# Kernel tuning notes

Hardware: AMD Instinct MI355X
Metric: run time of the kernel (lower is better)

## Reference

```python
import jax, jax.numpy as jnp
import numpy as np
from jax import lax

# pywt Wavelet('db4') decomposition filters
DEC_LO = jnp.array([-0.010597401784997278, 0.032883011666982945, 0.030841381835986965,
                    -0.18703481171888114, -0.02798376941698385, 0.6308807679295904,
                    0.7148465705525415, 0.23037781330885523], dtype=jnp.float32)
DEC_HI = jnp.array([-0.23037781330885523, 0.7148465705525415, -0.6308807679295904,
                    -0.02798376941698385, 0.18703481171888114, 0.030841381835986965,
                    -0.032883011666982945, -0.010597401784997278], dtype=jnp.float32)


def dwt_level(x, lo, hi):
    # single-level pywt dwt, mode='symmetric', along last axis
    f = lo.shape[0]
    p = f - 1
    pad = [(0, 0)] * (x.ndim - 1) + [(p, p)]
    xe = jnp.pad(x, pad, mode='symmetric')[..., 1:]  # offset 1 matches pywt phase
    lead = x.shape[:-1]
    xin = xe.reshape(-1, 1, xe.shape[-1])            # [N,1,L]
    filt = jnp.stack([lo[::-1], hi[::-1]])[:, None, :]  # flip: true convolution, [2,1,f]
    out = lax.conv_general_dilated(xin, filt, (2,), 'VALID')  # [N,2,floor((n+f-1)/2)]
    cA = out[:, 0].reshape(lead + (-1,))
    cD = out[:, 1].reshape(lead + (-1,))
    return cA, cD


def wavedec4(x):
    # pywt.wavedec(x,'db4',level=4) concatenated: [cA4,cD4,cD3,cD2,cD1]
    details = []
    a = x
    for _ in range(4):
        a, d = dwt_level(a, DEC_LO, DEC_HI)
        details.append(d)
    return jnp.concatenate([a] + details[::-1], axis=-1)


def lstm_last(xs, w_ih, w_hh, b_ih, b_hh):
    # torch LSTM (gate order i,f,g,o); returns last timestep hidden state
    B, T, _ = xs.shape
    H = w_hh.shape[1]
    h0 = jnp.zeros((B, H), xs.dtype)
    c0 = jnp.zeros((B, H), xs.dtype)
    b = b_ih + b_hh

    def step(carry, x_t):
        h, c = carry
        gates = x_t @ w_ih.T + h @ w_hh.T + b
        i, f, g, o = jnp.split(gates, 4, axis=-1)
        c = jax.nn.sigmoid(f) * c + jax.nn.sigmoid(i) * jnp.tanh(g)
        h = jax.nn.sigmoid(o) * jnp.tanh(c)
        return (h, c), None

    (h, _), _ = lax.scan(step, (h0, c0), jnp.swapaxes(xs, 0, 1))
    return h


def setup_inputs() -> dict:
    key = jax.random.key(0)
    ks = jax.random.split(key, 9)
    B, S, T = 256, 1024, 21
    return {
        'x': jax.random.normal(ks[0], (B, S, T), jnp.float32),
        'conv_w': jax.random.normal(ks[1], (64, 78, 3), jnp.float32) * 0.06,
        'conv_b': jax.random.normal(ks[2], (64,), jnp.float32) * 0.06,
        'w_ih': jax.random.normal(ks[3], (128, 64), jnp.float32) * 0.12,
        'w_hh': jax.random.normal(ks[4], (128, 32), jnp.float32) * 0.17,
        'b_ih': jax.random.normal(ks[5], (128,), jnp.float32) * 0.17,
        'b_hh': jax.random.normal(ks[6], (128,), jnp.float32) * 0.17,
        'fc_w': jax.random.normal(ks[7], (1, 32), jnp.float32) * 0.17,
        'fc_b': jax.random.normal(ks[8], (1,), jnp.float32) * 0.17,
    }


def reference(x, conv_w, conv_b, w_ih, w_hh, b_ih, b_hh, fc_w, fc_b):
    freq = jnp.abs(jnp.fft.rfft(x, axis=2))          # [B,S,11]
    tf = wavedec4(x)                                 # [B,S,46]
    combined = jnp.concatenate([x, freq, tf], axis=2)  # [B,S,78]
    combined = jnp.swapaxes(combined, 1, 2)          # [B,78,S]
    y = lax.conv_general_dilated(combined, conv_w, (1,), [(1, 1)]) + conv_b[None, :, None]
    y = jax.nn.relu(y)
    B, C, S = y.shape
    y = y.reshape(B, C, S // 2, 2).max(axis=-1)      # max_pool1d(k=2,s=2)
    y = jnp.transpose(y, (0, 2, 1))                  # [B,S//2,64]
    h = lstm_last(y, w_ih, w_hh, b_ih, b_hh)         # [B,32]
    return h @ fc_w.T + fc_b                         # [B,1]
```

## Files before the change

kernel.cpp:

```cpp
#include <hip/hip_runtime.h>
#include <math.h>

typedef _Float16 half8 __attribute__((ext_vector_type(8)));
typedef __fp16 fp16x2 __attribute__((ext_vector_type(2)));
typedef float floatx16 __attribute__((ext_vector_type(16)));
typedef float float2v __attribute__((ext_vector_type(2)));

constexpr float L2E = 1.4426950408889634f;

constexpr float DLO[8] = {-0.010597401784997278f, 0.032883011666982945f, 0.030841381835986965f,
                          -0.18703481171888114f, -0.02798376941698385f, 0.6308807679295904f,
                          0.7148465705525415f, 0.23037781330885523f};
constexpr float DHI[8] = {-0.23037781330885523f, 0.7148465705525415f, -0.6308807679295904f,
                          -0.02798376941698385f, 0.18703481171888114f, 0.030841381835986965f,
                          -0.032883011666982945f, -0.010597401784997278f};

constexpr float CT21[21] = {
  1.0f,          0.95557281f,  0.82623877f,  0.62348980f,  0.36534102f,  0.07473009f,
  -0.22252093f, -0.5f,        -0.73305187f, -0.90096887f, -0.98883083f,
  -0.98883083f, -0.90096887f, -0.73305187f, -0.5f,        -0.22252093f,
  0.07473009f,   0.36534102f,  0.62348980f,  0.82623877f,  0.95557281f};
constexpr float ST21[21] = {
  0.0f,          0.29475517f,  0.56332006f,  0.78183148f,  0.93087375f,  0.99720380f,
  0.97492791f,   0.86602540f,  0.68017274f,  0.43388374f,  0.14904227f,
  -0.14904227f, -0.43388374f, -0.68017274f, -0.86602540f, -0.97492791f,
  -0.99720380f, -0.93087375f, -0.78183148f, -0.56332006f, -0.29475517f};

template<int N>
__device__ __forceinline__ void dwt_step(const float* in, float* a, float* d) {
  constexpr int NO = (N + 7) / 2;
#pragma unroll
  for (int i = 0; i < NO; i++) {
    float sa = 0.f, sd = 0.f;
#pragma unroll
    for (int j = 0; j < 8; j++) {
      int rel = 2 * i + j - 6;
      int idx = (rel < 0) ? (-rel - 1) : ((rel >= N) ? (2 * N - rel - 1) : rel);
      float v = in[idx];
      sa = fmaf(v, DLO[7 - j], sa);
      sd = fmaf(v, DHI[7 - j], sd);
    }
    a[i] = sa;
    d[i] = sd;
  }
}

__device__ __forceinline__ void gload_lds16(const void* g, void* l) {
  __builtin_amdgcn_global_load_lds(
      (const __attribute__((address_space(1))) unsigned int*)g,
      (__attribute__((address_space(3))) unsigned int*)l, 16, 0, 0);
}

__device__ __forceinline__ void feature_row(const float* __restrict__ xr,
                                            _Float16* hrow) {
  float xx[21];
#pragma unroll
  for (int t = 0; t < 21; t++) xx[t] = xr[t];

#pragma unroll
  for (int i = 78; i < 88; i++) hrow[i] = (_Float16)0.f;

#pragma unroll
  for (int t = 0; t < 21; t++) hrow[t] = (_Float16)xx[t];

#pragma unroll
  for (int k = 0; k < 11; k++) {
    float re = 0.f, im = 0.f;
#pragma unroll
    for (int t = 0; t < 21; t++) {
      const int m = (k * t) % 21;
      re = fmaf(xx[t], CT21[m], re);
      im = fmaf(xx[t], ST21[m], im);
    }
    hrow[21 + k] = (_Float16)sqrtf(re * re + im * im);
  }

  float a1[14], d1[14];
  dwt_step<21>(xx, a1, d1);
#pragma unroll
  for (int i = 0; i < 14; i++) hrow[64 + i] = (_Float16)d1[i];
  float a2[10], d2[10];
  dwt_step<14>(a1, a2, d2);
#pragma unroll
  for (int i = 0; i < 10; i++) hrow[54 + i] = (_Float16)d2[i];
  float a3[8], d3[8];
  dwt_step<10>(a2, a3, d3);
#pragma unroll
  for (int i = 0; i < 8; i++) hrow[46 + i] = (_Float16)d3[i];
  float a4[7], d4[7];
  dwt_step<8>(a3, a4, d4);
#pragma unroll
  for (int i = 0; i < 7; i++) {
    hrow[32 + i] = (_Float16)a4[i];
    hrow[39 + i] = (_Float16)d4[i];
  }
}

__global__ __launch_bounds__(256) void wprep_kernel(const float* __restrict__ cw,
                                                    const float* __restrict__ w_ih,
                                                    const float* __restrict__ b_ih,
                                                    const float* __restrict__ b_hh,
                                                    _Float16* __restrict__ WbT,
                                                    _Float16* __restrict__ wih16,
                                                    float* __restrict__ biasI) {
  int idx = blockIdx.x * 256 + threadIdx.x;
  if (idx < 64 * 264) {
    int o = idx / 264, k = idx - o * 264;
    float v = 0.f;
    if (k < 240) {
      int dk = k / 80, c = k - dk * 80;
      if (c < 78) v = cw[o * 234 + c * 3 + dk];
    }
    WbT[idx] = (_Float16)v;
  } else if (idx < 16896 + 8192) {
    int j = idx - 16896;
    wih16[j] = (_Float16)(L2E * w_ih[j]);
  } else if (idx < 16896 + 8192 + 128) {
    int g = idx - 16896 - 8192;
    int p = ((g & 63) << 1) | (g >> 6);
    float s = (g < 64) ? 1.f : ((g < 96) ? 2.f : -1.f);
    biasI[p] = s * L2E * (b_ih[g] + b_hh[g]);
  }
}

__device__ __forceinline__ unsigned bcast_lane_u(unsigned v, int k) {
  return (unsigned)__builtin_amdgcn_readlane((int)v, k);
}

#if __has_builtin(__builtin_amdgcn_exp2f)
#define EXP2F __builtin_amdgcn_exp2f
#else
#define EXP2F exp2f
#endif

#if __has_builtin(__builtin_amdgcn_permlane32_swap)
__device__ __forceinline__ float swap_half(float x) {
  auto r = __builtin_amdgcn_permlane32_swap(__float_as_uint(x), __float_as_uint(x),
                                            false, false);
  return __uint_as_float(r[1]);
}
#else
__device__ __forceinline__ float swap_half(float x) { return __shfl_down(x, 32); }
#endif

__device__ __forceinline__ float dpp_swap1(float x) {
  int r = __builtin_amdgcn_update_dpp(0, __builtin_bit_cast(int, x),
                                      0xB1, 0xF, 0xF, true);
  return __builtin_bit_cast(float, r);
}

__device__ __forceinline__ unsigned pkrtz_u(float a, float b) {
  auto h = __builtin_amdgcn_cvt_pkrtz(a, b);
  return __builtin_bit_cast(unsigned, h);
}

__device__ __forceinline__ float fdot2u(unsigned a, unsigned b, float c) {
#if __has_builtin(__builtin_amdgcn_fdot2)
  return __builtin_amdgcn_fdot2(__builtin_bit_cast(fp16x2, a),
                                __builtin_bit_cast(fp16x2, b), c, false);
#else
  fp16x2 av = __builtin_bit_cast(fp16x2, a);
  fp16x2 bv = __builtin_bit_cast(fp16x2, b);
  return c + (float)av[0] * (float)bv[0] + (float)av[1] * (float)bv[1];
#endif
}

__device__ __forceinline__ void lstm_step(float& h, float& c, float2v xg,
                                          const unsigned* __restrict__ wA2,
                                          const unsigned* __restrict__ wB2,
                                          float mB, float aB) {
  unsigned q = pkrtz_u(h, dpp_swap1(h));
  unsigned hp[16];
#pragma unroll
  for (int m = 0; m < 16; m++) hp[m] = bcast_lane_u(q, 2 * m);

  float aA0 = xg.x, aA1 = 0.f, aB0 = xg.y, aB1 = 0.f;
#pragma unroll
  for (int m = 0; m < 8; m++) {
    aA0 = fdot2u(wA2[m], hp[m], aA0);
    aB0 = fdot2u(wB2[m], hp[m], aB0);
    aA1 = fdot2u(wA2[m + 8], hp[m + 8], aA1);
    aB1 = fdot2u(wB2[m + 8], hp[m + 8], aB1);
  }
  const float gA = aA0 + aA1;
  const float gB = aB0 + aB1;

  float rA = __builtin_amdgcn_rcpf(1.0f + EXP2F(-gA));
  float rB = __builtin_amdgcn_rcpf(EXP2F(gB) + 1.0f);
  float sB = fmaf(mB, rB, aB);

  float fv = swap_half(rA);
  float ov = swap_half(sB);
  c = fmaf(fv, c, rA * sB);
  float rc = __builtin_amdgcn_rcpf(EXP2F(c) + 1.0f);
  float ov2 = ov + ov;
  h = fmaf(-ov2, rc, ov);
}

__device__ __forceinline__ void prod_barrier(int* pb, int& target) {
  target += 3;
  __builtin_amdgcn_s_waitcnt(0);
  if ((threadIdx.x & 63) == 0)
    __hip_atomic_fetch_add(pb, 1, __ATOMIC_RELEASE, __HIP_MEMORY_SCOPE_WORKGROUP);
  while (__hip_atomic_load(pb, __ATOMIC_ACQUIRE, __HIP_MEMORY_SCOPE_WORKGROUP) < target) {
  }
}

__global__ __launch_bounds__(256, 1)
__attribute__((amdgpu_waves_per_eu(1, 1)))
void fused_kernel(const float* __restrict__ x,
                  const _Float16* __restrict__ WbT,
                  const float* __restrict__ cbias,
                  const _Float16* __restrict__ wih16,
                  const float* __restrict__ biasI,
                  const float* __restrict__ w_hh,
                  const float* __restrict__ fc_w,
                  const float* __restrict__ fc_b,
                  float* __restrict__ Xp,
                  float* __restrict__ out) {
  __shared__ __align__(16) char smem[61184];
  __shared__ int ready;
  __shared__ int pbar;
  _Float16* At = (_Float16*)smem;
  _Float16* Bt = (_Float16*)(smem + 24576);
  _Float16* yt = (_Float16*)smem;
  _Float16* wl = (_Float16*)(smem + 9216);
  float* biasl = (float*)(smem + 27648);
  float* Xpt   = (float*)(smem + 28160);
  float* bl    = (float*)(smem + 60928);

  const int tid = threadIdx.x;
  const int b = blockIdx.x;

  if (tid == 0) { ready = 0; pbar = 0; }
  if (tid < 64) bl[tid] = cbias[tid];
  __syncthreads();

  if (tid < 64) {
    const int L = tid;
    const bool lo = (L < 32);
    const float K = 2.0f * L2E;
    const float mB = lo ? -2.f * K : 1.f;
    const float aB = lo ? K : 0.f;
    const float sclB = L2E * (lo ? 2.f : -1.f);
    unsigned wA2[16], wB2[16];
    {
      const float4* rAp = (const float4*)(w_hh + L * 32);
      const float4* rBp = (const float4*)(w_hh + (L + 64) * 32);
#pragma unroll
      for (int q = 0; q < 8; q++) {
        float4 a4 = rAp[q], b4 = rBp[q];
        wA2[2 * q]     = pkrtz_u(L2E * a4.x, L2E * a4.y);
        wA2[2 * q + 1] = pkrtz_u(L2E * a4.z, L2E * a4.w);
        wB2[2 * q]     = pkrtz_u(sclB * b4.x, sclB * b4.y);
        wB2[2 * q + 1] = pkrtz_u(sclB * b4.z, sclB * b4.w);
      }
    }

    float h = 0.f, c = 0.f;
    for (int k = 0; k < 8; k++) {
      while (__hip_atomic_load(&ready, __ATOMIC_ACQUIRE, __HIP_MEMORY_SCOPE_WORKGROUP) < k + 1)
        __builtin_amdgcn_s_sleep(2);
      const float* xp = Xp + ((size_t)b * 512 + (size_t)k * 64) * 128;
      float2v p2[4];
#pragma unroll
      for (int u = 0; u < 4; u++) p2[u] = *(const float2v*)&xp[u * 128 + 2 * L];
      for (int t0 = 0; t0 < 64; t0 += 4) {
        float2v c2[4];
#pragma unroll
        for (int u = 0; u < 4; u++) c2[u] = p2[u];
        if (t0 + 4 < 64) {
#pragma unroll
          for (int u = 0; u < 4; u++)
            p2[u] = *(const float2v*)&xp[(t0 + 4 + u) * 128 + 2 * L];
        }
#pragma unroll
        for (int u = 0; u < 4; u++)
          lstm_step(h, c, c2[u], wA2, wB2, mB, aB);
      }
    }

    float v = lo ? h * fc_w[L & 31] : 0.f;
#pragma unroll
    for (int off = 32; off > 0; off >>= 1) v += __shfl_down(v, off);
    if (L == 0) out[b] = v + fc_b[0];
  } else {
    const int ptid = tid - 64;
    const int pw = (tid >> 6) - 1;
    const int lane = tid & 63, ml = lane & 31, kg = lane >> 5;
    int bt = 0;

    for (int k = 0; k < 8; k++) {
      const int s0 = k * 128;

      {
        const char* srcB = (const char*)WbT;
#pragma unroll
        for (int j = 0; j < 11; j++) {
          const int idx = j * 192 + ptid;
          gload_lds16(srcB + (size_t)idx * 16, (char*)Bt + (size_t)idx * 16);
        }
      }
      if (ptid < 130) {
        const int s = s0 - 1 + ptid;
        __align__(16) _Float16 hrow[88];
        if (s < 0 || s > 1023) {
#pragma unroll
          for (int i = 0; i < 88; i++) hrow[i] = (_Float16)0.f;
        } else {
          feature_row(x + ((size_t)(b << 10) + s) * 21, hrow);
        }
        uint4* dst = (uint4*)&At[ptid * 88];
        const uint4* src = (const uint4*)hrow;
#pragma unroll
        for (int i = 0; i < 11; i++) dst[i] = src[i];
      }
      prod_barrier(&pbar, bt);

      float pooled[3][8];
      {
        int cc = 0;
        for (int wt = pw; wt < 8; wt += 3, cc++) {
          const int mt = wt & 3, nt = wt >> 2;
          floatx16 acc = {};
#pragma unroll
          for (int ks = 0; ks < 15; ks++) {
            const int kb = ks * 16 + kg * 8;
            const int dk = (kb >= 160) ? 2 : ((kb >= 80) ? 1 : 0);
            const int cofs = kb - dk * 80;
            half8 av = *(const half8*)&At[(mt * 32 + ml + dk) * 88 + cofs];
            half8 bv = *(const half8*)&Bt[(nt * 32 + ml) * 264 + kb];
            acc = __builtin_amdgcn_mfma_f32_32x32x16_f16(av, bv, acc, 0, 0, 0);
          }
          const float bo = bl[nt * 32 + ml];
#pragma unroll
          for (int p = 0; p < 8; p++)
            pooled[cc][p] = fmaxf(fmaxf(acc[2 * p], acc[2 * p + 1]) + bo, 0.f);
        }
      }
      prod_barrier(&pbar, bt);

      {
        int cc = 0;
        for (int wt = pw; wt < 8; wt += 3, cc++) {
          const int mt = wt & 3, nt = wt >> 2;
#pragma unroll
          for (int p = 0; p < 8; p++) {
            const int toff = (p & 1) + ((p >> 1) << 2);
            const int t = mt * 16 + (kg << 1) + toff;
            yt[t * 72 + nt * 32 + ml] = (_Float16)pooled[cc][p];
          }
        }
        for (int i = ptid; i < 2048; i += 192) {
          int g = i >> 4, c4 = i & 15;
          *(uint2*)(wl + g * 72 + c4 * 4) = *(const uint2*)(wih16 + g * 64 + c4 * 4);
        }
        if (ptid < 128) biasl[ptid] = biasI[ptid];
      }
      prod_barrier(&pbar, bt);

      for (int wt = pw; wt < 8; wt += 3) {
        const int pm = wt & 1, pn = wt >> 1;
        floatx16 pa = {};
#pragma unroll
        for (int kq = 0; kq < 4; kq++) {
          const int k0 = kq * 16 + kg * 8;
          half8 av = *(const half8*)&yt[(pm * 32 + ml) * 72 + k0];
          half8 bv = *(const half8*)&wl[(pn * 32 + ml) * 72 + k0];
          pa = __builtin_amdgcn_mfma_f32_32x32x16_f16(av, bv, pa, 0, 0, 0);
        }
        const int gi = pn * 32 + ml;
        const int pp = ((gi & 63) << 1) | (gi >> 6);
#pragma unroll
        for (int reg = 0; reg < 16; reg++) {
          const int row = (reg & 3) + 8 * (reg >> 2) + 4 * kg;
          Xpt[(pm * 32 + row) * 128 + pp] = pa[reg];
        }
      }
      prod_barrier(&pbar, bt);

      {
        float* xpg = Xp + ((size_t)b * 512 + (size_t)k * 64) * 128;
        for (int i = ptid; i < 2048; i += 192) {
          const int r = i >> 5, c4 = (i & 31) << 2;
          const float sOdd = (c4 < 64) ? 2.f : -1.f;
          float4 v = *(float4*)&Xpt[r * 128 + c4];
          float4 bb = *(float4*)&biasl[c4];
          v.x += bb.x; v.y = fmaf(v.y, sOdd, bb.y);
          v.z += bb.z; v.w = fmaf(v.w, sOdd, bb.w);
          *(float4*)&xpg[r * 128 + c4] = v;
        }
      }
      prod_barrier(&pbar, bt);

      if (tid == 64)
        __hip_atomic_fetch_add(&ready, 1, __ATOMIC_RELEASE, __HIP_MEMORY_SCOPE_WORKGROUP);
    }
  }
}

extern "C" void kernel_launch(void* const* d_in, const int* in_sizes, int n_in,
                              void* d_out, int out_size, void* d_ws, size_t ws_size,
                              hipStream_t stream) {
  const float* x      = (const float*)d_in[0];
  const float* conv_w = (const float*)d_in[1];
  const float* conv_b = (const float*)d_in[2];
  const float* w_ih   = (const float*)d_in[3];
  const float* w_hh   = (const float*)d_in[4];
  const float* b_ih   = (const float*)d_in[5];
  const float* b_hh   = (const float*)d_in[6];
  const float* fc_w   = (const float*)d_in[7];
  const float* fc_b   = (const float*)d_in[8];
  float* out = (float*)d_out;

  char* wsb = (char*)d_ws;
  float*    Xp    = (float*)wsb;
  _Float16* WbT   = (_Float16*)(wsb + 67108864);
  _Float16* wih16 = (_Float16*)(wsb + 67108864 + 33792);
  float*    biasI = (float*)(wsb + 67108864 + 33792 + 16384);

  wprep_kernel<<<dim3(99), dim3(256), 0, stream>>>(conv_w, w_ih, b_ih, b_hh,
                                                   WbT, wih16, biasI);
  fused_kernel<<<dim3(256), dim3(256), 0, stream>>>(x, WbT, conv_b, wih16, biasI,
                                                    w_hh, fc_w, fc_b, Xp, out);
}
```

Measured before the change: 184.2 us.

## Fold weight preparation into fused kernel and keep weights resident in LDS

Removes the separate weight-prep kernel launch. Each block now converts the conv and LSTM input weights and the biases to fp16 in LDS once, before its chunk loop, instead of reloading preprocessed weights from global memory every chunk. LDS grows so the weights stay resident, and the LSTM recurrent dot product uses four independent accumulator chains instead of two to shorten the dependency chain. The risks are redundant per-block conversion work at kernel start and a larger LDS footprint, although occupancy is already fixed at one block.

Measured after the change: 203.8 us. 1.11x slower.

```diff
diff --git a/kernel.cpp b/kernel.cpp
--- a/kernel.cpp
+++ b/kernel.cpp
@@ -45,12 +45,6 @@
   }
 }
 
-__device__ __forceinline__ void gload_lds16(const void* g, void* l) {
-  __builtin_amdgcn_global_load_lds(
-      (const __attribute__((address_space(1))) unsigned int*)g,
-      (__attribute__((address_space(3))) unsigned int*)l, 16, 0, 0);
-}
-
 __device__ __forceinline__ void feature_row(const float* __restrict__ xr,
                                             _Float16* hrow) {
   float xx[21];
@@ -93,33 +87,6 @@
   for (int i = 0; i < 7; i++) {
     hrow[32 + i] = (_Float16)a4[i];
     hrow[39 + i] = (_Float16)d4[i];
-  }
-}
-
-__global__ __launch_bounds__(256) void wprep_kernel(const float* __restrict__ cw,
-                                                    const float* __restrict__ w_ih,
-                                                    const float* __restrict__ b_ih,
-                                                    const float* __restrict__ b_hh,
-                                                    _Float16* __restrict__ WbT,
-                                                    _Float16* __restrict__ wih16,
-                                                    float* __restrict__ biasI) {
-  int idx = blockIdx.x * 256 + threadIdx.x;
-  if (idx < 64 * 264) {
-    int o = idx / 264, k = idx - o * 264;
-    float v = 0.f;
-    if (k < 240) {
-      int dk = k / 80, c = k - dk * 80;
-      if (c < 78) v = cw[o * 234 + c * 3 + dk];
-    }
-    WbT[idx] = (_Float16)v;
-  } else if (idx < 16896 + 8192) {
-    int j = idx - 16896;
-    wih16[j] = (_Float16)(L2E * w_ih[j]);
-  } else if (idx < 16896 + 8192 + 128) {
-    int g = idx - 16896 - 8192;
-    int p = ((g & 63) << 1) | (g >> 6);
-    float s = (g < 64) ? 1.f : ((g < 96) ? 2.f : -1.f);
-    biasI[p] = s * L2E * (b_ih[g] + b_hh[g]);
   }
 }
 
@@ -174,16 +141,21 @@
 #pragma unroll
   for (int m = 0; m < 16; m++) hp[m] = bcast_lane_u(q, 2 * m);
 
-  float aA0 = xg.x, aA1 = 0.f, aB0 = xg.y, aB1 = 0.f;
-#pragma unroll
-  for (int m = 0; m < 8; m++) {
-    aA0 = fdot2u(wA2[m], hp[m], aA0);
-    aB0 = fdot2u(wB2[m], hp[m], aB0);
-    aA1 = fdot2u(wA2[m + 8], hp[m + 8], aA1);
-    aB1 = fdot2u(wB2[m + 8], hp[m + 8], aB1);
-  }
-  const float gA = aA0 + aA1;
-  const float gB = aB0 + aB1;
+  float A0 = xg.x, A1 = 0.f, A2 = 0.f, A3 = 0.f;
+  float B0 = xg.y, B1 = 0.f, B2 = 0.f, B3 = 0.f;
+#pragma unroll
+  for (int m = 0; m < 4; m++) {
+    A0 = fdot2u(wA2[m], hp[m], A0);
+    B0 = fdot2u(wB2[m], hp[m], B0);
+    A1 = fdot2u(wA2[m + 4], hp[m + 4], A1);
+    B1 = fdot2u(wB2[m + 4], hp[m + 4], B1);
+    A2 = fdot2u(wA2[m + 8], hp[m + 8], A2);
+    B2 = fdot2u(wB2[m + 8], hp[m + 8], B2);
+    A3 = fdot2u(wA2[m + 12], hp[m + 12], A3);
+    B3 = fdot2u(wB2[m + 12], hp[m + 12], B3);
+  }
+  const float gA = (A0 + A1) + (A2 + A3);
+  const float gB = (B0 + B1) + (B2 + B3);
 
   float rA = __builtin_amdgcn_rcpf(1.0f + EXP2F(-gA));
   float rB = __builtin_amdgcn_rcpf(EXP2F(gB) + 1.0f);
@@ -209,25 +181,26 @@
 __global__ __launch_bounds__(256, 1)
 __attribute__((amdgpu_waves_per_eu(1, 1)))
 void fused_kernel(const float* __restrict__ x,
-                  const _Float16* __restrict__ WbT,
+                  const float* __restrict__ cw,
                   const float* __restrict__ cbias,
-                  const _Float16* __restrict__ wih16,
-                  const float* __restrict__ biasI,
+                  const float* __restrict__ w_ih,
+                  const float* __restrict__ b_ih,
+                  const float* __restrict__ b_hh,
                   const float* __restrict__ w_hh,
                   const float* __restrict__ fc_w,
                   const float* __restrict__ fc_b,
                   float* __restrict__ Xp,
                   float* __restrict__ out) {
-  __shared__ __align__(16) char smem[61184];
+  __shared__ __align__(16) char smem[110336];
   __shared__ int ready;
   __shared__ int pbar;
   _Float16* At = (_Float16*)smem;
+  _Float16* yt = (_Float16*)smem;
   _Float16* Bt = (_Float16*)(smem + 24576);
-  _Float16* yt = (_Float16*)smem;
-  _Float16* wl = (_Float16*)(smem + 9216);
-  float* biasl = (float*)(smem + 27648);
-  float* Xpt   = (float*)(smem + 28160);
-  float* bl    = (float*)(smem + 60928);
+  _Float16* wl = (_Float16*)(smem + 58368);
+  float* Xpt   = (float*)(smem + 76800);
+  float* biasl = (float*)(smem + 109568);
+  float* bl    = (float*)(smem + 110080);
 
   const int tid = threadIdx.x;
   const int b = blockIdx.x;
@@ -290,17 +263,28 @@
     const int lane = tid & 63, ml = lane & 31, kg = lane >> 5;
     int bt = 0;
 
+    for (int i = ptid; i < 16896; i += 192) {
+      const int o = i / 264, k2 = i - o * 264;
+      float v = 0.f;
+      if (k2 < 240) {
+        const int dk = k2 / 80, cc = k2 - dk * 80;
+        if (cc < 78) v = cw[o * 234 + cc * 3 + dk];
+      }
+      Bt[i] = (_Float16)v;
+    }
+    for (int i = ptid; i < 8192; i += 192) {
+      const int g = i >> 6, j = i & 63;
+      wl[g * 72 + j] = (_Float16)(L2E * w_ih[i]);
+    }
+    for (int g = ptid; g < 128; g += 192) {
+      const int p = ((g & 63) << 1) | (g >> 6);
+      const float s = (g < 64) ? 1.f : ((g < 96) ? 2.f : -1.f);
+      biasl[p] = s * L2E * (b_ih[g] + b_hh[g]);
+    }
+
     for (int k = 0; k < 8; k++) {
       const int s0 = k * 128;
 
-      {
-        const char* srcB = (const char*)WbT;
-#pragma unroll
-        for (int j = 0; j < 11; j++) {
-          const int idx = j * 192 + ptid;
-          gload_lds16(srcB + (size_t)idx * 16, (char*)Bt + (size_t)idx * 16);
-        }
-      }
       if (ptid < 130) {
         const int s = s0 - 1 + ptid;
         __align__(16) _Float16 hrow[88];
@@ -351,11 +335,6 @@
             yt[t * 72 + nt * 32 + ml] = (_Float16)pooled[cc][p];
           }
         }
-        for (int i = ptid; i < 2048; i += 192) {
-          int g = i >> 4, c4 = i & 15;
-          *(uint2*)(wl + g * 72 + c4 * 4) = *(const uint2*)(wih16 + g * 64 + c4 * 4);
-        }
-        if (ptid < 128) biasl[ptid] = biasI[ptid];
       }
       prod_barrier(&pbar, bt);
 
@@ -413,14 +392,9 @@
   const float* fc_b   = (const float*)d_in[8];
   float* out = (float*)d_out;
 
-  char* wsb = (char*)d_ws;
-  float*    Xp    = (float*)wsb;
-  _Float16* WbT   = (_Float16*)(wsb + 67108864);
-  _Float16* wih16 = (_Float16*)(wsb + 67108864 + 33792);
-  float*    biasI = (float*)(wsb + 67108864 + 33792 + 16384);
-
-  wprep_kernel<<<dim3(99), dim3(256), 0, stream>>>(conv_w, w_ih, b_ih, b_hh,
-                                                   WbT, wih16, biasI);
-  fused_kernel<<<dim3(256), dim3(256), 0, stream>>>(x, WbT, conv_b, wih16, biasI,
-                                                    w_hh, fc_w, fc_b, Xp, out);
-}
+  float* Xp = (float*)d_ws;
+
+  fused_kernel<<<dim3(256), dim3(256), 0, stream>>>(x, conv_w, conv_b, w_ih,
+                                                    b_ih, b_hh, w_hh, fc_w, fc_b,
+                                                    Xp, out);
+}
```
